# Performance work log

Measured on AMD Instinct MI355X. Metric: run time of the kernel, lower is better.

The kernel has to match this reference:

```python
import jax, jax.numpy as jnp
import numpy as np

# SMPL kinematic tree (24 joints)
PARENTS = [-1, 0, 0, 0, 1, 2, 3, 4, 5, 6, 7, 8, 9, 9, 9, 12, 13, 14, 16, 17, 18, 19, 20, 21]
B, V, J, NB = 1024, 6890, 24, 10
POSE_BASIS = 9 * (J - 1)  # 207


def setup_inputs() -> dict:
    key = jax.random.key(0)
    ks = jax.random.split(key, 8)
    betas = jax.random.normal(ks[0], (B, NB), jnp.float32)
    global_rot = jax.random.normal(ks[1], (B, 1, 3, 3), jnp.float32)
    body_pose = jax.random.normal(ks[2], (B, J - 1, 3, 3), jnp.float32)
    v_template = jax.random.normal(ks[3], (V, 3), jnp.float32)
    shapedirs = jax.random.normal(ks[4], (V, 3, NB), jnp.float32) * 0.01
    posedirs = jax.random.normal(ks[5], (POSE_BASIS, V * 3), jnp.float32) * 0.01
    J_regressor = jax.random.uniform(ks[6], (J, V), jnp.float32) / V
    w = jax.random.uniform(ks[7], (V, J), jnp.float32)
    lbs_weights = w / w.sum(-1, keepdims=True)
    return dict(betas=betas, global_rot=global_rot, body_pose=body_pose,
                v_template=v_template, shapedirs=shapedirs, posedirs=posedirs,
                J_regressor=J_regressor, lbs_weights=lbs_weights)


def reference(betas, global_rot, body_pose, v_template, shapedirs, posedirs,
              J_regressor, lbs_weights):
    b = betas.shape[0]
    full_pose = jnp.concatenate([global_rot, body_pose], axis=1)  # [B,24,3,3]

    # shape blend shapes
    v_shaped = v_template + jnp.einsum('bl,vcl->bvc', betas, shapedirs)  # [B,V,3]
    Jt = jnp.einsum('jv,bvc->bjc', J_regressor, v_shaped)  # [B,24,3]

    # pose blend shapes (pose2rot=False: rotations given)
    eye3 = jnp.eye(3, dtype=betas.dtype)
    pose_feature = (full_pose[:, 1:] - eye3).reshape(b, POSE_BASIS)  # [B,207]
    v_posed = v_shaped + (pose_feature @ posedirs).reshape(b, V, 3)

    # forward kinematics along parent chain
    rel_joints = jnp.concatenate(
        [Jt[:, :1], Jt[:, 1:] - Jt[:, jnp.array(PARENTS[1:])]], axis=1)  # [B,24,3]
    top = jnp.concatenate([full_pose, rel_joints[..., None]], axis=-1)  # [B,24,3,4]
    bottom = jnp.broadcast_to(jnp.array([0., 0., 0., 1.], dtype=betas.dtype),
                              (b, J, 1, 4))
    T_local = jnp.concatenate([top, bottom], axis=-2)  # [B,24,4,4]

    chain = [T_local[:, 0]]
    for i in range(1, J):  # fixed small tree, sequential dependency
        chain.append(chain[PARENTS[i]] @ T_local[:, i])
    A = jnp.stack(chain, axis=1)  # [B,24,4,4]

    posed_joints = A[..., :3, 3]  # [B,24,3]
    # make transforms relative to rest-pose joints
    rel_t = posed_joints - jnp.einsum('bjmn,bjn->bjm', A[..., :3, :3], Jt)
    A_rel = A.at[..., :3, 3].set(rel_t)

    # linear blend skinning
    T = jnp.einsum('vj,bjmn->bvmn', lbs_weights, A_rel)  # [B,V,4,4]
    vertices = jnp.einsum('bvmn,bvn->bvm', T[..., :3, :3], v_posed) + T[..., :3, 3]
    return vertices, posed_joints
```

## Files before the change

### kernel.cpp

```cpp
#include <hip/hip_runtime.h>

#define BN 1024
#define NV 6890
#define NBETA 10
#define PB 207
#define N3 20670
#define NCOL 20736
#define NCHUNK 7
#define BT 32

typedef __bf16 bf16x8 __attribute__((ext_vector_type(8)));
typedef float  f32x4  __attribute__((ext_vector_type(4)));

__device__ __constant__ int c_par[24] = {-1,0,0,0,1,2,3,4,5,6,7,8,9,9,9,12,13,14,16,17,18,19,20,21};

__device__ inline unsigned short f2bf(float f) {
    unsigned u = __float_as_uint(f);
    u += 0x7fff + ((u >> 16) & 1);
    return (unsigned short)(u >> 16);
}

__device__ inline void dma16(const void* g, void* l) {
    __builtin_amdgcn_global_load_lds(
        (const __attribute__((address_space(1))) unsigned int*)g,
        (__attribute__((address_space(3))) unsigned int*)l, 16, 0, 0);
}

__global__ __launch_bounds__(256) void k_prep(const float* __restrict__ pd,
                                              const float* __restrict__ sd,
                                              const float* __restrict__ vtm,
                                              const float* __restrict__ Jr,
                                              const float* __restrict__ bpose,
                                              const float* __restrict__ betas,
                                              const float* __restrict__ w,
                                              unsigned short* __restrict__ ws_pdt,
                                              unsigned short* __restrict__ ws_pfb,
                                              unsigned short* __restrict__ ws_wb,
                                              float* __restrict__ ws_jsp)
{
    int blk = blockIdx.x;
    if (blk < 567) {
        int t = blk * 256 + threadIdx.x;
        int kc = t / NCOL;
        int col = t - kc * NCOL;
        bool cok = col < N3;
        unsigned short vals[40];
        #pragma unroll
        for (int kk = 0; kk < 32; kk++) {
            int gk = kc * 32 + kk;
            float val = 0.f;
            if (cok) {
                if (gk < PB)             val = pd[(size_t)gk * N3 + col];
                else if (gk < PB + 10)   val = sd[(size_t)col * NBETA + (gk - PB)];
                else if (gk == PB + 10)  val = vtm[col];
            }
            vals[kk] = f2bf(val);
        }
        #pragma unroll
        for (int kk = 32; kk < 40; kk++) vals[kk] = 0;
        uint4* dst = (uint4*)(ws_pdt + (size_t)t * 40);
        #pragma unroll
        for (int q = 0; q < 5; q++) {
            uint4 u;
            u.x = vals[q*8+0] | ((unsigned)vals[q*8+1] << 16);
            u.y = vals[q*8+2] | ((unsigned)vals[q*8+3] << 16);
            u.z = vals[q*8+4] | ((unsigned)vals[q*8+5] << 16);
            u.w = vals[q*8+6] | ((unsigned)vals[q*8+7] << 16);
            dst[q] = u;
        }
    } else if (blk < 799) {
        int e0 = (blk - 567) * 1024 + threadIdx.x * 4;
        unsigned short v4[4];
        #pragma unroll
        for (int r = 0; r < 4; r++) {
            int e = e0 + r;
            int b = e / 232, k = e - b * 232;
            float x = 0.f;
            if (k < PB) {
                x = bpose[(size_t)b * PB + k];
                int k9 = k % 9;
                if (k9 == 0 || k9 == 4 || k9 == 8) x -= 1.f;
            } else if (k < PB + 10) {
                x = betas[b * NBETA + (k - PB)];
            } else if (k == PB + 10) {
                x = 1.f;
            }
            v4[r] = f2bf(x);
        }
        uint2 u;
        u.x = v4[0] | ((unsigned)v4[1] << 16);
        u.y = v4[2] | ((unsigned)v4[3] << 16);
        *(uint2*)(ws_pfb + e0) = u;
    } else if (blk < 1069) {
        int e0 = (blk - 799) * 1024 + threadIdx.x * 4;
        unsigned short v4[4];
        #pragma unroll
        for (int r = 0; r < 4; r++) {
            int e = e0 + r;
            int v = e / 40, j = e - v * 40;
            float val = (j < 24 && v < NV) ? w[(size_t)v * 24 + j] : 0.f;
            v4[r] = f2bf(val);
        }
        uint2 u;
        u.x = v4[0] | ((unsigned)v4[1] << 16);
        u.y = v4[2] | ((unsigned)v4[3] << 16);
        *(uint2*)(ws_wb + e0) = u;
    } else {
        int b2 = blk - 1069;
        int jc = b2 >> 3;
        int seg = b2 & 7;
        int j = jc / 3, c = jc % 3;
        int v0 = seg * 862;
        int v1 = v0 + 862; if (v1 > NV) v1 = NV;

        float acc[11];
        #pragma unroll
        for (int l = 0; l < 11; l++) acc[l] = 0.f;

        for (int v = v0 + threadIdx.x; v < v1; v += 256) {
            float r = Jr[j * NV + v];
            acc[10] += r * vtm[v * 3 + c];
            const float* s = sd + (size_t)(v * 3 + c) * NBETA;
            #pragma unroll
            for (int l = 0; l < NBETA; l++) acc[l] += r * s[l];
        }

        __shared__ float red[4][11];
        int lane = threadIdx.x & 63, wv = threadIdx.x >> 6;
        #pragma unroll
        for (int l = 0; l < 11; l++) {
            float x = acc[l];
            x += __shfl_down(x, 32, 64);
            x += __shfl_down(x, 16, 64);
            x += __shfl_down(x, 8, 64);
            x += __shfl_down(x, 4, 64);
            x += __shfl_down(x, 2, 64);
            x += __shfl_down(x, 1, 64);
            if (lane == 0) red[wv][l] = x;
        }
        __syncthreads();
        if (threadIdx.x == 0) {
            #pragma unroll
            for (int l = 0; l < 11; l++)
                ws_jsp[((size_t)seg * 72 + jc) * 11 + l]
                    = red[0][l] + red[1][l] + red[2][l] + red[3][l];
        }
    }
}

__global__ __launch_bounds__(256) void k_chain(const float* __restrict__ betas,
                                               const float* __restrict__ grot,
                                               const float* __restrict__ bpose,
                                               const float* __restrict__ ws_jsp,
                                               unsigned short* __restrict__ ws_artb,
                                               float* __restrict__ pj)
{
    __shared__ float js_s[72 * 11];
    __shared__ float jt[16][72];
    __shared__ float tl[16][288];
    __shared__ float am[16][288];
    int tid = threadIdx.x;

    for (int e = tid; e < 72 * 11; e += 256) {
        float s = 0.f;
        #pragma unroll
        for (int seg = 0; seg < 8; seg++)
            s += ws_jsp[(size_t)seg * 792 + e];
        js_s[e] = s;
    }
    __syncthreads();

    int lb = tid >> 4;
    int e  = tid & 15;
    int b  = blockIdx.x * 16 + lb;

    for (int idx = e; idx < 72; idx += 16) {
        float acc = js_s[idx * 11 + 10];
        const float* be = betas + b * NBETA;
        #pragma unroll
        for (int l = 0; l < NBETA; l++) acc += be[l] * js_s[idx * 11 + l];
        jt[lb][idx] = acc;
    }
    __syncthreads();

    for (int idx = e; idx < 288; idx += 16) {
        int j = idx / 12, e12 = idx % 12, m = e12 >> 2, n = e12 & 3;
        float val;
        if (n < 3) {
            val = (j == 0) ? grot[(size_t)b * 9 + m * 3 + n]
                           : bpose[((size_t)b * 23 + (j - 1)) * 9 + m * 3 + n];
        } else {
            val = jt[lb][j * 3 + m];
            if (j > 0) val -= jt[lb][c_par[j] * 3 + m];
        }
        tl[lb][idx] = val;
    }
    __syncthreads();

    if (e < 12) am[lb][e] = tl[lb][e];
    for (int i = 1; i < 24; i++) {
        __syncthreads();
        if (e < 12) {
            int p = c_par[i];
            int m = e >> 2, n = e & 3;
            float val = am[lb][p*12 + m*4 + 0] * tl[lb][i*12 + 0 + n]
                      + am[lb][p*12 + m*4 + 1] * tl[lb][i*12 + 4 + n]
                      + am[lb][p*12 + m*4 + 2] * tl[lb][i*12 + 8 + n];
            if (n == 3) val += am[lb][p*12 + m*4 + 3];
            am[lb][i*12 + e] = val;
        }
    }
    __syncthreads();

    for (int idx = e; idx < 72; idx += 16) {
        int j = idx / 3, m = idx % 3;
        pj[(size_t)b * 72 + idx] = am[lb][j*12 + m*4 + 3];
    }
    for (int idx = e; idx < 480; idx += 16) {
        int col = idx / 40, j = idx - col * 40;
        float val = 0.f;
        if (j < 24) {
            int m = col >> 2, n = col & 3;
            if (n < 3) {
                val = am[lb][j*12 + col];
            } else {
                val = am[lb][j*12 + m*4 + 3]
                    - am[lb][j*12 + m*4 + 0] * jt[lb][j*3 + 0]
                    - am[lb][j*12 + m*4 + 1] * jt[lb][j*3 + 1]
                    - am[lb][j*12 + m*4 + 2] * jt[lb][j*3 + 2];
            }
        }
        ws_artb[(size_t)b * 480 + idx] = f2bf(val);
    }
}

__global__ __launch_bounds__(256, 4) void k_vert(const unsigned short* __restrict__ ws_pdt,
                                                 const unsigned short* __restrict__ ws_pfb,
                                                 const unsigned short* __restrict__ ws_wb,
                                                 const unsigned short* __restrict__ ws_artb,
                                                 float* __restrict__ out)
{
    const int bb = blockIdx.x;
    const int vb = blockIdx.y;
    const int tid = threadIdx.x;
    const int wv = tid >> 6;
    const int lane = tid & 63;
    const int r16 = lane & 15;
    const int half8 = (lane >> 4) * 8;

    __shared__ __align__(16) unsigned char smem[40448];
    unsigned short* pdT_l = (unsigned short*)smem;
    float*          disp_l = (float*)smem;
    unsigned short* ArT_l = (unsigned short*)(smem + 25088);

    {
        const unsigned short* srcA = ws_artb + (size_t)(bb * BT) * 480;
        for (int i = wv; i < 15; i += 4)
            dma16((const char*)srcA + i * 1024 + lane * 16, (char*)ArT_l + i * 1024);
        const unsigned short* srcP = ws_pdt + (size_t)vb * 192 * 40;
        for (int i = wv; i < 15; i += 4)
            dma16((const char*)srcP + i * 1024 + lane * 16, (char*)pdT_l + i * 1024);
    }

    const unsigned short* pfbase = ws_pfb + (size_t)(bb * BT) * 232;
    bf16x8 a0 = *(const bf16x8*)(pfbase + r16 * 232 + half8);
    bf16x8 a1 = *(const bf16x8*)(pfbase + (16 + r16) * 232 + half8);

    __syncthreads();

    f32x4 acc[2][3];
    #pragma unroll
    for (int mt = 0; mt < 2; mt++)
        #pragma unroll
        for (int t = 0; t < 3; t++)
            acc[mt][t] = (f32x4){0.f, 0.f, 0.f, 0.f};

    #pragma unroll
    for (int kc = 0; kc < NCHUNK; kc++) {
        bf16x8 b0 = *(const bf16x8*)(pdT_l + (wv * 48 + r16) * 40 + half8);
        bf16x8 b1 = *(const bf16x8*)(pdT_l + (wv * 48 + 16 + r16) * 40 + half8);
        bf16x8 b2 = *(const bf16x8*)(pdT_l + (wv * 48 + 32 + r16) * 40 + half8);
        bf16x8 a0n, a1n;
        if (kc < NCHUNK - 1) {
            a0n = *(const bf16x8*)(pfbase + r16 * 232 + (kc + 1) * 32 + half8);
            a1n = *(const bf16x8*)(pfbase + (16 + r16) * 232 + (kc + 1) * 32 + half8);
        }
        __syncthreads();
        if (kc < NCHUNK - 1) {
            const unsigned short* src = ws_pdt + ((size_t)(kc + 1) * NCOL + (size_t)vb * 192) * 40;
            for (int i = wv; i < 15; i += 4)
                dma16((const char*)src + i * 1024 + lane * 16, (char*)pdT_l + i * 1024);
        }
        acc[0][0] = __builtin_amdgcn_mfma_f32_16x16x32_bf16(a0, b0, acc[0][0], 0, 0, 0);
        acc[1][0] = __builtin_amdgcn_mfma_f32_16x16x32_bf16(a1, b0, acc[1][0], 0, 0, 0);
        acc[0][1] = __builtin_amdgcn_mfma_f32_16x16x32_bf16(a0, b1, acc[0][1], 0, 0, 0);
        acc[1][1] = __builtin_amdgcn_mfma_f32_16x16x32_bf16(a1, b1, acc[1][1], 0, 0, 0);
        acc[0][2] = __builtin_amdgcn_mfma_f32_16x16x32_bf16(a0, b2, acc[0][2], 0, 0, 0);
        acc[1][2] = __builtin_amdgcn_mfma_f32_16x16x32_bf16(a1, b2, acc[1][2], 0, 0, 0);
        a0 = a0n; a1 = a1n;
        if (kc < NCHUNK - 1) __syncthreads();
    }

    #pragma unroll
    for (int mt = 0; mt < 2; mt++) {
        #pragma unroll
        for (int t = 0; t < 3; t++) {
            int col = wv * 48 + t * 16 + r16;
            int brow = mt * 16 + (lane >> 4) * 4;
            #pragma unroll
            for (int r = 0; r < 4; r++)
                disp_l[(brow + r) * 196 + col] = acc[mt][t][r];
        }
    }
    __syncthreads();

    bf16x8 aw = *(const bf16x8*)(ws_wb + (size_t)(vb * 64 + wv * 16 + r16) * 40 + half8);

    const int g = lane >> 4;
    const int v16 = wv * 16 + r16;
    const int vg = vb * 64 + v16;
    int bl[3], mm[3];
    #pragma unroll
    for (int t = 0; t < 3; t++) {
        int q = 4 * t + g;
        bl[t] = (q * 11) >> 5;
        mm[t] = q - 3 * bl[t];
    }

    for (int half = 0; half < 2; half++) {
        if (half == 1) {
            __syncthreads();
            const unsigned short* srcA = ws_artb + (size_t)(bb * BT + 16) * 480;
            for (int i = wv; i < 15; i += 4)
                dma16((const char*)srcA + i * 1024 + lane * 16, (char*)ArT_l + i * 1024);
            __syncthreads();
        }
        for (int s = 0; s < 4; s++) {
            int sub = half * 4 + s;
            bf16x8 bA0 = *(const bf16x8*)(ArT_l + (s * 48 + r16) * 40 + half8);
            bf16x8 bA1 = *(const bf16x8*)(ArT_l + (s * 48 + 16 + r16) * 40 + half8);
            bf16x8 bA2 = *(const bf16x8*)(ArT_l + (s * 48 + 32 + r16) * 40 + half8);
            f32x4 z = (f32x4){0.f, 0.f, 0.f, 0.f};
            f32x4 t0 = __builtin_amdgcn_mfma_f32_16x16x32_bf16(bA0, aw, z, 0, 0, 0);
            f32x4 t1 = __builtin_amdgcn_mfma_f32_16x16x32_bf16(bA1, aw, z, 0, 0, 0);
            f32x4 t2 = __builtin_amdgcn_mfma_f32_16x16x32_bf16(bA2, aw, z, 0, 0, 0);

            #pragma unroll
            for (int t = 0; t < 3; t++) {
                f32x4 tt = (t == 0) ? t0 : (t == 1) ? t1 : t2;
                int row = sub * 4 + bl[t];
                const float* d = disp_l + row * 196 + v16 * 3;
                float x = d[0], y = d[1], zz = d[2];
                float p = tt[0] * x + tt[1] * y + tt[2] * zz + tt[3];
                if (vg < NV)
                    out[(size_t)(bb * BT + row) * N3 + (size_t)vg * 3 + mm[t]] = p;
            }
        }
    }
}

extern "C" void kernel_launch(void* const* d_in, const int* in_sizes, int n_in,
                              void* d_out, int out_size, void* d_ws, size_t ws_size,
                              hipStream_t stream) {
    const float* betas = (const float*)d_in[0];
    const float* grot  = (const float*)d_in[1];
    const float* bpose = (const float*)d_in[2];
    const float* vtm   = (const float*)d_in[3];
    const float* sd    = (const float*)d_in[4];
    const float* pd    = (const float*)d_in[5];
    const float* Jr    = (const float*)d_in[6];
    const float* w     = (const float*)d_in[7];
    float* out = (float*)d_out;

    char* ws = (char*)d_ws;
    unsigned short* ws_pdt  = (unsigned short*)(ws);
    unsigned short* ws_pfb  = (unsigned short*)(ws + 11612160);
    unsigned short* ws_wb   = (unsigned short*)(ws + 12087296);
    float*          ws_jsp  = (float*)         (ws + 12640256);
    unsigned short* ws_artb = (unsigned short*)(ws + 12665600);

    k_prep<<<1645, 256, 0, stream>>>(pd, sd, vtm, Jr, bpose, betas, w,
                                     ws_pdt, ws_pfb, ws_wb, ws_jsp);
    k_chain<<<BN / 16, 256, 0, stream>>>(betas, grot, bpose, ws_jsp, ws_artb,
                                         out + (size_t)BN * N3);
    k_vert<<<dim3(32, 108), 256, 0, stream>>>(ws_pdt, ws_pfb, ws_wb, ws_artb, out);
}
```

Baseline: 180.2 us.

## Load MFMA operands directly from global into registers, dropping LDS staging

```diff
diff --git a/kernel.cpp b/kernel.cpp
--- a/kernel.cpp
+++ b/kernel.cpp
@@ -18,12 +18,6 @@
     unsigned u = __float_as_uint(f);
     u += 0x7fff + ((u >> 16) & 1);
     return (unsigned short)(u >> 16);
-}
-
-__device__ inline void dma16(const void* g, void* l) {
-    __builtin_amdgcn_global_load_lds(
-        (const __attribute__((address_space(1))) unsigned int*)g,
-        (__attribute__((address_space(3))) unsigned int*)l, 16, 0, 0);
 }
 
 __global__ __launch_bounds__(256) void k_prep(const float* __restrict__ pd,
@@ -248,25 +242,16 @@
     const int r16 = lane & 15;
     const int half8 = (lane >> 4) * 8;
 
-    __shared__ __align__(16) unsigned char smem[40448];
-    unsigned short* pdT_l = (unsigned short*)smem;
-    float*          disp_l = (float*)smem;
-    unsigned short* ArT_l = (unsigned short*)(smem + 25088);
-
-    {
-        const unsigned short* srcA = ws_artb + (size_t)(bb * BT) * 480;
-        for (int i = wv; i < 15; i += 4)
-            dma16((const char*)srcA + i * 1024 + lane * 16, (char*)ArT_l + i * 1024);
-        const unsigned short* srcP = ws_pdt + (size_t)vb * 192 * 40;
-        for (int i = wv; i < 15; i += 4)
-            dma16((const char*)srcP + i * 1024 + lane * 16, (char*)pdT_l + i * 1024);
-    }
+    __shared__ __align__(16) float disp_l[32 * 196];
 
     const unsigned short* pfbase = ws_pfb + (size_t)(bb * BT) * 232;
+    const unsigned short* pB0 = ws_pdt + ((size_t)vb * 192 + wv * 48 + r16) * 40 + half8;
+
     bf16x8 a0 = *(const bf16x8*)(pfbase + r16 * 232 + half8);
     bf16x8 a1 = *(const bf16x8*)(pfbase + (16 + r16) * 232 + half8);
-
-    __syncthreads();
+    bf16x8 b0 = *(const bf16x8*)(pB0);
+    bf16x8 b1 = *(const bf16x8*)(pB0 + 640);
+    bf16x8 b2 = *(const bf16x8*)(pB0 + 1280);
 
     f32x4 acc[2][3];
     #pragma unroll
@@ -277,19 +262,14 @@
 
     #pragma unroll
     for (int kc = 0; kc < NCHUNK; kc++) {
-        bf16x8 b0 = *(const bf16x8*)(pdT_l + (wv * 48 + r16) * 40 + half8);
-        bf16x8 b1 = *(const bf16x8*)(pdT_l + (wv * 48 + 16 + r16) * 40 + half8);
-        bf16x8 b2 = *(const bf16x8*)(pdT_l + (wv * 48 + 32 + r16) * 40 + half8);
-        bf16x8 a0n, a1n;
+        bf16x8 a0n, a1n, b0n, b1n, b2n;
         if (kc < NCHUNK - 1) {
+            const unsigned short* pn = pB0 + (size_t)(kc + 1) * NCOL * 40;
+            b0n = *(const bf16x8*)(pn);
+            b1n = *(const bf16x8*)(pn + 640);
+            b2n = *(const bf16x8*)(pn + 1280);
             a0n = *(const bf16x8*)(pfbase + r16 * 232 + (kc + 1) * 32 + half8);
             a1n = *(const bf16x8*)(pfbase + (16 + r16) * 232 + (kc + 1) * 32 + half8);
-        }
-        __syncthreads();
-        if (kc < NCHUNK - 1) {
-            const unsigned short* src = ws_pdt + ((size_t)(kc + 1) * NCOL + (size_t)vb * 192) * 40;
-            for (int i = wv; i < 15; i += 4)
-                dma16((const char*)src + i * 1024 + lane * 16, (char*)pdT_l + i * 1024);
         }
         acc[0][0] = __builtin_amdgcn_mfma_f32_16x16x32_bf16(a0, b0, acc[0][0], 0, 0, 0);
         acc[1][0] = __builtin_amdgcn_mfma_f32_16x16x32_bf16(a1, b0, acc[1][0], 0, 0, 0);
@@ -297,8 +277,7 @@
         acc[1][1] = __builtin_amdgcn_mfma_f32_16x16x32_bf16(a1, b1, acc[1][1], 0, 0, 0);
         acc[0][2] = __builtin_amdgcn_mfma_f32_16x16x32_bf16(a0, b2, acc[0][2], 0, 0, 0);
         acc[1][2] = __builtin_amdgcn_mfma_f32_16x16x32_bf16(a1, b2, acc[1][2], 0, 0, 0);
-        a0 = a0n; a1 = a1n;
-        if (kc < NCHUNK - 1) __syncthreads();
+        if (kc < NCHUNK - 1) { a0 = a0n; a1 = a1n; b0 = b0n; b1 = b1n; b2 = b2n; }
     }
 
     #pragma unroll
@@ -327,35 +306,37 @@
         mm[t] = q - 3 * bl[t];
     }
 
-    for (int half = 0; half < 2; half++) {
-        if (half == 1) {
-            __syncthreads();
-            const unsigned short* srcA = ws_artb + (size_t)(bb * BT + 16) * 480;
-            for (int i = wv; i < 15; i += 4)
-                dma16((const char*)srcA + i * 1024 + lane * 16, (char*)ArT_l + i * 1024);
-            __syncthreads();
-        }
-        for (int s = 0; s < 4; s++) {
-            int sub = half * 4 + s;
-            bf16x8 bA0 = *(const bf16x8*)(ArT_l + (s * 48 + r16) * 40 + half8);
-            bf16x8 bA1 = *(const bf16x8*)(ArT_l + (s * 48 + 16 + r16) * 40 + half8);
-            bf16x8 bA2 = *(const bf16x8*)(ArT_l + (s * 48 + 32 + r16) * 40 + half8);
-            f32x4 z = (f32x4){0.f, 0.f, 0.f, 0.f};
-            f32x4 t0 = __builtin_amdgcn_mfma_f32_16x16x32_bf16(bA0, aw, z, 0, 0, 0);
-            f32x4 t1 = __builtin_amdgcn_mfma_f32_16x16x32_bf16(bA1, aw, z, 0, 0, 0);
-            f32x4 t2 = __builtin_amdgcn_mfma_f32_16x16x32_bf16(bA2, aw, z, 0, 0, 0);
-
-            #pragma unroll
-            for (int t = 0; t < 3; t++) {
-                f32x4 tt = (t == 0) ? t0 : (t == 1) ? t1 : t2;
-                int row = sub * 4 + bl[t];
-                const float* d = disp_l + row * 196 + v16 * 3;
-                float x = d[0], y = d[1], zz = d[2];
-                float p = tt[0] * x + tt[1] * y + tt[2] * zz + tt[3];
-                if (vg < NV)
-                    out[(size_t)(bb * BT + row) * N3 + (size_t)vg * 3 + mm[t]] = p;
-            }
-        }
+    const unsigned short* pArt = ws_artb + (size_t)(bb * BT) * 480 + (size_t)r16 * 40 + half8;
+
+    bf16x8 c0 = *(const bf16x8*)(pArt);
+    bf16x8 c1 = *(const bf16x8*)(pArt + 640);
+    bf16x8 c2 = *(const bf16x8*)(pArt + 1280);
+
+    #pragma unroll
+    for (int sub = 0; sub < 8; sub++) {
+        bf16x8 c0n, c1n, c2n;
+        if (sub < 7) {
+            const unsigned short* pn = pArt + (size_t)(sub + 1) * 1920;
+            c0n = *(const bf16x8*)(pn);
+            c1n = *(const bf16x8*)(pn + 640);
+            c2n = *(const bf16x8*)(pn + 1280);
+        }
+        f32x4 z = (f32x4){0.f, 0.f, 0.f, 0.f};
+        f32x4 t0 = __builtin_amdgcn_mfma_f32_16x16x32_bf16(c0, aw, z, 0, 0, 0);
+        f32x4 t1 = __builtin_amdgcn_mfma_f32_16x16x32_bf16(c1, aw, z, 0, 0, 0);
+        f32x4 t2 = __builtin_amdgcn_mfma_f32_16x16x32_bf16(c2, aw, z, 0, 0, 0);
+
+        #pragma unroll
+        for (int t = 0; t < 3; t++) {
+            f32x4 tt = (t == 0) ? t0 : (t == 1) ? t1 : t2;
+            int row = sub * 4 + bl[t];
+            const float* d = disp_l + row * 196 + v16 * 3;
+            float x = d[0], y = d[1], zz = d[2];
+            float p = tt[0] * x + tt[1] * y + tt[2] * zz + tt[3];
+            if (vg < NV)
+                out[(size_t)(bb * BT + row) * N3 + (size_t)vg * 3 + mm[t]] = p;
+        }
+        if (sub < 7) { c0 = c0n; c1 = c1n; c2 = c2n; }
     }
 }
 
```

New measurement: 183.9 us. +2.0%, slower.
